# Kernel optimization log

Hardware: AMD Instinct MI355X
Metric: run time of the kernel (lower is better)

## Reference

```python
import jax, jax.numpy as jnp
import numpy as np

SQRT2 = np.float32(np.sqrt(2.0))


def _depthwise(x, h, axis):
    """Symmetric-pad depthwise 1D conv along `axis` (2=col/height, 3=row/width).
    Emulates dtcwt_slim ColFilter/RowFilter: prep_filt flips the taps, then
    F.conv2d cross-correlates with groups=C (same taps for every channel).
    x: (B,C,H,W), h: (L,) with L odd -> same-size output."""
    C = x.shape[1]
    L = h.shape[0]
    m = L // 2
    hf = jnp.flip(h)  # prep_filt stores h[::-1]
    if axis == 2:
        xp = jnp.pad(x, ((0, 0), (0, 0), (m, m), (0, 0)), mode='symmetric')
        ker = jnp.tile(hf[None, None, :, None], (C, 1, 1, 1))  # (C,1,L,1)
    else:
        xp = jnp.pad(x, ((0, 0), (0, 0), (0, 0), (m, m)), mode='symmetric')
        ker = jnp.tile(hf[None, None, None, :], (C, 1, 1, 1))  # (C,1,1,L)
    return jax.lax.conv_general_dilated(
        xp, ker, window_strides=(1, 1), padding='VALID',
        dimension_numbers=('NCHW', 'OIHW', 'NCHW'), feature_group_count=C)


def colfilter(x, h):
    return _depthwise(x, h, axis=2)


def rowfilter(x, h):
    return _depthwise(x, h, axis=3)


def c2q(w_r, w_i):
    """Complex pair of subbands -> real quad-interleaved image.
    w_r, w_i: (B,C,2,H,W) -> (B,C,2H,2W)."""
    w1r, w1i = w_r[:, :, 0], w_i[:, :, 0]
    w2r, w2i = w_r[:, :, 1], w_i[:, :, 1]
    x1 = w1r + w2r          # y[::2,  ::2]
    x2 = w1i + w2i          # y[::2, 1::2]
    x3 = w1i - w2i          # y[1::2, ::2]
    x4 = w2r - w1r          # y[1::2,1::2]
    B, C, H, W = x1.shape
    top = jnp.stack([x1, x2], axis=-1).reshape(B, C, H, 2 * W)
    bot = jnp.stack([x3, x4], axis=-1).reshape(B, C, H, 2 * W)
    y = jnp.stack([top, bot], axis=-2).reshape(B, C, 2 * H, 2 * W)
    return y / SQRT2


def setup_inputs() -> dict:
    key = jax.random.key(0)
    k1, k2, k3, k4, k5, k6 = jax.random.split(key, 6)
    B, C, H, W = 8, 64, 256, 256
    Yl = jax.random.normal(k1, (B, C, H, W), dtype=jnp.float32)
    Yhr = jax.random.normal(k2, (B, C, 6, H // 2, W // 2), dtype=jnp.float32)
    Yhi = jax.random.normal(k3, (B, C, 6, H // 2, W // 2), dtype=jnp.float32)
    # near_sym_b_bp synthesis filters (fixed, non-trainable buffers): 13/19/13 taps
    g0o = jax.random.normal(k4, (13,), dtype=jnp.float32) * 0.3
    g1o = jax.random.normal(k5, (19,), dtype=jnp.float32) * 0.3
    g2o = jax.random.normal(k6, (13,), dtype=jnp.float32) * 0.3
    return {"Yl": Yl, "Yhr": Yhr, "Yhi": Yhi, "g0o": g0o, "g1o": g1o, "g2o": g2o}


def reference(Yl, Yhr, Yhi, g0o, g1o, g2o):
    # orientation pairs: (15,165)->lh uses bands 0,5; (75,105)->hl bands 2,3;
    # (45,135 bandpass)->hh bands 1,4
    lh = c2q(Yhr[:, :, 0:6:5], Yhi[:, :, 0:6:5])
    hl = c2q(Yhr[:, :, 2:4:1], Yhi[:, :, 2:4:1])
    hh = c2q(Yhr[:, :, 1:5:3], Yhi[:, :, 1:5:3])
    y1 = colfilter(Yl, g0o) + colfilter(lh, g1o)
    y2 = colfilter(hl, g0o)
    y2bp = colfilter(hh, g2o)
    y = rowfilter(y1, g0o) + rowfilter(y2, g1o) + rowfilter(y2bp, g2o)
    return y
```

## Files before the change

### kernel.cpp

```cpp
#include <hip/hip_runtime.h>

#define PW 90
#define IS2 0.70710678118654752f

__device__ __forceinline__ int symidx(int t, int n) {
    t = (t < 0) ? (-1 - t) : t;
    return (t >= n) ? (2 * n - 1 - t) : t;
}

#define SB() __builtin_amdgcn_sched_barrier(0)

__device__ __forceinline__ void col13_yl(
    float (&acc)[32], const float* __restrict__ ylp,
    const float* __restrict__ taps, int r0, int cc)
{
    #pragma unroll
    for (int pi = 0; pi < 44; ++pi) {
        int rr = symidx(r0 - 6 + pi, 256);
        float v = ylp[rr * 256 + cc];
        #pragma unroll
        for (int j = 0; j < 13; ++j) {
            int ro = pi + j - 12;
            if (ro >= 0 && ro < 32) acc[ro] = fmaf(taps[j], v, acc[ro]);
        }
    }
}

__device__ __forceinline__ void col13_c2q(
    float (&acc)[32], const float* __restrict__ yhr, const float* __restrict__ yhi,
    int bA, int bB, const float* __restrict__ taps, int r0, int cc)
{
    const int cp = cc & 1;
    const int j2 = cc >> 1;
    #pragma unroll
    for (int pi = 0; pi < 44; ++pi) {
        int rr = symidx(r0 - 6 + pi, 256);
        int rp = rr & 1;
        int i2 = rr >> 1;
        const float* base = (((rp ^ cp) != 0) ? yhi : yhr) + (i2 * 128 + j2);
        float A  = base[bA * 16384];
        float Bv = base[bB * 16384];
        float vA = (rp & cp)       ? -A  : A;
        float vB = (rp & (cp ^ 1)) ? -Bv : Bv;
        float v = (vA + vB) * IS2;
        #pragma unroll
        for (int j = 0; j < 13; ++j) {
            int ro = pi + j - 12;
            if (ro >= 0 && ro < 32) acc[ro] = fmaf(taps[j], v, acc[ro]);
        }
    }
}

__device__ __forceinline__ void col19_c2q(
    float (&acc)[32], const float* __restrict__ yhr, const float* __restrict__ yhi,
    const float* __restrict__ taps, int r0, int cc)
{
    const int bA = 0, bB = 5;
    const int cp = cc & 1;
    const int j2 = cc >> 1;
    #pragma unroll
    for (int pi = 0; pi < 50; ++pi) {
        int rr = symidx(r0 - 9 + pi, 256);
        int rp = rr & 1;
        int i2 = rr >> 1;
        const float* base = (((rp ^ cp) != 0) ? yhi : yhr) + (i2 * 128 + j2);
        float A  = base[bA * 16384];
        float Bv = base[bB * 16384];
        float vA = (rp & cp)       ? -A  : A;
        float vB = (rp & (cp ^ 1)) ? -Bv : Bv;
        float v = (vA + vB) * IS2;
        #pragma unroll
        for (int j = 0; j < 19; ++j) {
            int ro = pi + j - 18;
            if (ro >= 0 && ro < 32) acc[ro] = fmaf(taps[j], v, acc[ro]);
        }
    }
}

template<int NU>
__device__ __forceinline__ void load_pairs(float (&buf)[28],
    const float* __restrict__ pEA, const float* __restrict__ pEB,
    const float* __restrict__ pOA, const float* __restrict__ pOB,
    int vof)
{
    #pragma unroll
    for (int u = 0; u < NU; ++u) {
        buf[4*u+0] = pEA[vof + u * 128];
        buf[4*u+1] = pEB[vof + u * 128];
        buf[4*u+2] = pOA[vof + u * 128];
        buf[4*u+3] = pOB[vof + u * 128];
    }
}

template<int L, int EPI0, int UB, int NU>
__device__ __forceinline__ void consume_pairs(float (&acc)[32], const float (&buf)[28],
                                              float sgn, const float* __restrict__ taps)
{
    #pragma unroll
    for (int u = 0; u < NU; ++u) {
        float ve = (buf[4*u+0] + buf[4*u+1]) * IS2;
        float vo = (buf[4*u+2] - buf[4*u+3]) * sgn;
        const int pi = EPI0 + 2 * (UB + u);
        #pragma unroll
        for (int j = 0; j < L; ++j) {
            int ro = pi + j - (L - 1);
            if (ro >= 0 && ro < 32) acc[ro] = fmaf(taps[j], ve, acc[ro]);
        }
        #pragma unroll
        for (int j = 0; j < L; ++j) {
            int ro = pi + 1 + j - (L - 1);
            if (ro >= 0 && ro < 32) acc[ro] = fmaf(taps[j], vo, acc[ro]);
        }
    }
}

template<int NT>
__device__ __forceinline__ void load_rows(float (&buf)[11], const float* __restrict__ p, int t0)
{
    #pragma unroll
    for (int t = 0; t < NT; ++t) buf[t] = p[(t0 + t) * 256];
}

template<int TB, int NT>
__device__ __forceinline__ void consume_rows(float (&acc)[32], const float (&buf)[11],
                                             const float* __restrict__ taps)
{
    #pragma unroll
    for (int t = 0; t < NT; ++t) {
        float v = buf[t];
        const int pi = TB + t;
        #pragma unroll
        for (int j = 0; j < 13; ++j) {
            int ro = pi + j - 12;
            if (ro >= 0 && ro < 32) acc[ro] = fmaf(taps[j], v, acc[ro]);
        }
    }
}

template<int L, int EPI0, int NPT, int C>
__device__ __forceinline__ void c2q_col_pipe(
    float (&acc)[32],
    const float* __restrict__ pEA, const float* __restrict__ pEB,
    const float* __restrict__ pOA, const float* __restrict__ pOB,
    int vof, float sgn, const float* __restrict__ taps)
{
    float bufA[28], bufB[28];
    constexpr int R = NPT - 3 * C;
    load_pairs<C>(bufA, pEA, pEB, pOA, pOB, vof);
    SB();
    load_pairs<C>(bufB, pEA, pEB, pOA, pOB, vof + C * 128);
    SB();
    consume_pairs<L, EPI0, 0, C>(acc, bufA, sgn, taps);
    SB();
    load_pairs<C>(bufA, pEA, pEB, pOA, pOB, vof + 2 * C * 128);
    SB();
    consume_pairs<L, EPI0, C, C>(acc, bufB, sgn, taps);
    SB();
    load_pairs<R>(bufB, pEA, pEB, pOA, pOB, vof + 3 * C * 128);
    SB();
    consume_pairs<L, EPI0, 2 * C, C>(acc, bufA, sgn, taps);
    SB();
    consume_pairs<L, EPI0, 3 * C, R>(acc, bufB, sgn, taps);
}

extern "C" __global__ __launch_bounds__(512, 4) void dtcwt_inv(
    const float* __restrict__ Yl, const float* __restrict__ Yhr,
    const float* __restrict__ Yhi,
    const float* __restrict__ g0, const float* __restrict__ g1,
    const float* __restrict__ g2, float* __restrict__ out)
{
    __shared__ __align__(16) float sU[3][32][PW];

    const int tid = threadIdx.x;
    const int wg  = blockIdx.x;
    const int swz = (wg & 7) * 2048 + (wg >> 3);
    const int plane = swz >> 5;
    const int bt = swz & 31;
    const int bx = bt & 3;
    const int by = bt >> 2;
    const int r0 = by * 32;
    const int c0 = bx * 64;

    const float* ylp = Yl  + (size_t)plane * 65536;
    const float* yhr = Yhr + (size_t)plane * 6 * 16384;
    const float* yhi = Yhi + (size_t)plane * 6 * 16384;

    const bool rowInterior = (by >= 1) && (by <= 6);

    const int role = tid >> 7;
    const int lr   = tid & 127;

    float acc[32];
    #pragma unroll
    for (int i = 0; i < 32; ++i) acc[i] = 0.0f;
    int ti = -1;

    if (rowInterior) {
        if (role == 0) {
            if (lr < 76) {
                ti = lr + 6;
                int cc = symidx(c0 + lr - 6, 256);
                const float* p = ylp + (r0 - 6) * 256 + cc;
                float bufA[11], bufB[11];
                load_rows<11>(bufA, p, 0);
                SB();
                load_rows<11>(bufB, p, 11);
                SB();
                consume_rows<0, 11>(acc, bufA, g0);
                SB();
                load_rows<11>(bufA, p, 22);
                SB();
                consume_rows<11, 11>(acc, bufB, g0);
                SB();
                load_rows<11>(bufB, p, 33);
                SB();
                consume_rows<22, 11>(acc, bufA, g0);
                SB();
                consume_rows<33, 11>(acc, bufB, g0);
            }
        } else if (role == 1) {
            if (lr < 76) {
                ti = lr + 6;
                int cc = symidx(c0 + lr - 6, 256);
                int cp = cc & 1, j2 = cc >> 1;
                const float* pE = cp ? yhi : yhr;
                const float* pO = cp ? yhr : yhi;
                float sgn = cp ? -IS2 : IS2;
                int vof = ((r0 - 10) >> 1) * 128 + j2;
                c2q_col_pipe<19, -1, 26, 7>(acc,
                    pE + 0 * 16384, pE + 5 * 16384,
                    pO + 0 * 16384, pO + 5 * 16384, vof, sgn, g1);
            }
        } else if (role == 2) {
            if (lr < 82) {
                ti = lr + 3;
                int cc = symidx(c0 + lr - 9, 256);
                int cp = cc & 1, j2 = cc >> 1;
                const float* pE = cp ? yhi : yhr;
                const float* pO = cp ? yhr : yhi;
                float sgn = cp ? -IS2 : IS2;
                int vof = ((r0 - 6) >> 1) * 128 + j2;
                c2q_col_pipe<13, 0, 22, 6>(acc,
                    pE + 2 * 16384, pE + 3 * 16384,
                    pO + 2 * 16384, pO + 3 * 16384, vof, sgn, g0);
            }
        } else {
            if (lr < 76) {
                ti = lr + 6;
                int cc = symidx(c0 + lr - 6, 256);
                int cp = cc & 1, j2 = cc >> 1;
                const float* pE = cp ? yhi : yhr;
                const float* pO = cp ? yhr : yhi;
                float sgn = cp ? -IS2 : IS2;
                int vof = ((r0 - 6) >> 1) * 128 + j2;
                c2q_col_pipe<13, 0, 22, 6>(acc,
                    pE + 1 * 16384, pE + 4 * 16384,
                    pO + 1 * 16384, pO + 4 * 16384, vof, sgn, g2);
            }
        }
    } else {
        if (role == 0) {
            if (lr < 76) {
                ti = lr + 6;
                int cc = symidx(c0 + ti - 12, 256);
                col13_yl(acc, ylp, g0, r0, cc);
            }
        } else if (role == 1) {
            if (lr < 76) {
                ti = lr + 6;
                int cc = symidx(c0 + ti - 12, 256);
                col19_c2q(acc, yhr, yhi, g1, r0, cc);
            }
        } else if (role == 2) {
            if (lr < 82) {
                ti = lr + 3;
                int cc = symidx(c0 + ti - 12, 256);
                col13_c2q(acc, yhr, yhi, 2, 3, g0, r0, cc);
            }
        } else {
            if (lr < 76) {
                ti = lr + 6;
                int cc = symidx(c0 + ti - 12, 256);
                col13_c2q(acc, yhr, yhi, 1, 4, g2, r0, cc);
            }
        }
    }

    if (ti >= 0 && role != 1) {
        const int bi = (role == 0) ? 0 : (role == 2 ? 1 : 2);
        #pragma unroll
        for (int ro = 0; ro < 32; ++ro) sU[bi][ro][ti] = acc[ro];
    }
    __syncthreads();

    if (role == 1 && ti >= 0) {
        #pragma unroll
        for (int ro = 0; ro < 32; ++ro) sU[0][ro][ti] += acc[ro];
    }

    const int cg = tid & 15;
    const int r2 = tid >> 4;
    const int cb = 4 * cg;

    float w2[28];
    #pragma unroll
    for (int k = 0; k < 14; ++k) {
        float2 a = *(const float2*)&sU[1][r2][cb + 2 * k];
        w2[2*k] = a.x; w2[2*k+1] = a.y;
    }
    float w3[20];
    #pragma unroll
    for (int k = 0; k < 10; ++k) {
        float2 a = *(const float2*)&sU[2][r2][cb + 4 + 2 * k];
        w3[2*k] = a.x; w3[2*k+1] = a.y;
    }
    __syncthreads();

    float w1[20];
    #pragma unroll
    for (int k = 0; k < 10; ++k) {
        float2 a = *(const float2*)&sU[0][r2][cb + 4 + 2 * k];
        w1[2*k] = a.x; w1[2*k+1] = a.y;
    }

    float4 res;
    float* op = (float*)&res;
    #pragma unroll
    for (int q = 0; q < 4; ++q) {
        float s = 0.0f;
        #pragma unroll
        for (int j = 0; j < 13; ++j) s = fmaf(g0[j], w1[q + 14 - j], s);
        #pragma unroll
        for (int j = 0; j < 19; ++j) s = fmaf(g1[j], w2[q + 21 - j], s);
        #pragma unroll
        for (int j = 0; j < 13; ++j) s = fmaf(g2[j], w3[q + 14 - j], s);
        op[q] = s;
    }
    *(float4*)&out[(size_t)plane * 65536 + (size_t)(r0 + r2) * 256 + (c0 + cb)] = res;
}

extern "C" void kernel_launch(void* const* d_in, const int* in_sizes, int n_in,
                              void* d_out, int out_size, void* d_ws, size_t ws_size,
                              hipStream_t stream) {
    const float* Yl  = (const float*)d_in[0];
    const float* Yhr = (const float*)d_in[1];
    const float* Yhi = (const float*)d_in[2];
    const float* g0  = (const float*)d_in[3];
    const float* g1  = (const float*)d_in[4];
    const float* g2  = (const float*)d_in[5];
    float* out = (float*)d_out;

    dim3 grid(16384, 1, 1);
    dim3 block(512, 1, 1);
    dtcwt_inv<<<grid, block, 0, stream>>>(Yl, Yhr, Yhi, g0, g1, g2, out);
}
```

Baseline: 312.6 us.

## Shrink tiles to 32x32, split 19-tap column pass across two waves

Output tiles shrink from 32x64 to 32x32, so the grid doubles and blocks drop from 512 to 320 threads, five 64-lane waves with one subband role each. The 19-tap lh column filter is split by input row range across two waves, which merge their partials into shared memory with atomicAdd. Shared buffers are resized per subband. The aim is better lane utilisation and balance across waves, at the cost of more halo recomputation per output pixel and idle threads in the row pass.

```diff
diff --git a/kernel.cpp b/kernel.cpp
--- a/kernel.cpp
+++ b/kernel.cpp
@@ -1,6 +1,7 @@
 #include <hip/hip_runtime.h>
 
-#define PW 90
+#define P1 46
+#define P2 52
 #define IS2 0.70710678118654752f
 
 __device__ __forceinline__ int symidx(int t, int n) {
@@ -51,21 +52,21 @@
     }
 }
 
-__device__ __forceinline__ void col19_c2q(
+template<int PI0, int PI1>
+__device__ __forceinline__ void col19_c2q_rng(
     float (&acc)[32], const float* __restrict__ yhr, const float* __restrict__ yhi,
     const float* __restrict__ taps, int r0, int cc)
 {
-    const int bA = 0, bB = 5;
     const int cp = cc & 1;
     const int j2 = cc >> 1;
     #pragma unroll
-    for (int pi = 0; pi < 50; ++pi) {
+    for (int pi = PI0; pi < PI1; ++pi) {
         int rr = symidx(r0 - 9 + pi, 256);
         int rp = rr & 1;
         int i2 = rr >> 1;
         const float* base = (((rp ^ cp) != 0) ? yhi : yhr) + (i2 * 128 + j2);
-        float A  = base[bA * 16384];
-        float Bv = base[bB * 16384];
+        float A  = base[0 * 16384];
+        float Bv = base[5 * 16384];
         float vA = (rp & cp)       ? -A  : A;
         float vB = (rp & (cp ^ 1)) ? -Bv : Bv;
         float v = (vA + vB) * IS2;
@@ -78,7 +79,7 @@
 }
 
 template<int NU>
-__device__ __forceinline__ void load_pairs(float (&buf)[28],
+__device__ __forceinline__ void load_pairs(float* buf,
     const float* __restrict__ pEA, const float* __restrict__ pEB,
     const float* __restrict__ pOA, const float* __restrict__ pOB,
     int vof)
@@ -93,7 +94,7 @@
 }
 
 template<int L, int EPI0, int UB, int NU>
-__device__ __forceinline__ void consume_pairs(float (&acc)[32], const float (&buf)[28],
+__device__ __forceinline__ void consume_pairs(float (&acc)[32], const float* buf,
                                               float sgn, const float* __restrict__ taps)
 {
     #pragma unroll
@@ -114,72 +115,75 @@
     }
 }
 
-template<int NT>
-__device__ __forceinline__ void load_rows(float (&buf)[11], const float* __restrict__ p, int t0)
-{
-    #pragma unroll
-    for (int t = 0; t < NT; ++t) buf[t] = p[(t0 + t) * 256];
-}
-
-template<int TB, int NT>
-__device__ __forceinline__ void consume_rows(float (&acc)[32], const float (&buf)[11],
-                                             const float* __restrict__ taps)
-{
-    #pragma unroll
-    for (int t = 0; t < NT; ++t) {
-        float v = buf[t];
-        const int pi = TB + t;
-        #pragma unroll
-        for (int j = 0; j < 13; ++j) {
-            int ro = pi + j - 12;
-            if (ro >= 0 && ro < 32) acc[ro] = fmaf(taps[j], v, acc[ro]);
-        }
-    }
-}
-
-template<int L, int EPI0, int NPT, int C>
+template<int L, int EPI0, int UOFF, int NPT, int C>
 __device__ __forceinline__ void c2q_col_pipe(
     float (&acc)[32],
     const float* __restrict__ pEA, const float* __restrict__ pEB,
     const float* __restrict__ pOA, const float* __restrict__ pOB,
     int vof, float sgn, const float* __restrict__ taps)
 {
-    float bufA[28], bufB[28];
+    float bufA[4 * C], bufB[4 * C];
     constexpr int R = NPT - 3 * C;
+    static_assert(R > 0 && R <= C, "chunking");
     load_pairs<C>(bufA, pEA, pEB, pOA, pOB, vof);
     SB();
     load_pairs<C>(bufB, pEA, pEB, pOA, pOB, vof + C * 128);
     SB();
-    consume_pairs<L, EPI0, 0, C>(acc, bufA, sgn, taps);
+    consume_pairs<L, EPI0, UOFF + 0, C>(acc, bufA, sgn, taps);
     SB();
     load_pairs<C>(bufA, pEA, pEB, pOA, pOB, vof + 2 * C * 128);
     SB();
-    consume_pairs<L, EPI0, C, C>(acc, bufB, sgn, taps);
+    consume_pairs<L, EPI0, UOFF + C, C>(acc, bufB, sgn, taps);
     SB();
     load_pairs<R>(bufB, pEA, pEB, pOA, pOB, vof + 3 * C * 128);
     SB();
-    consume_pairs<L, EPI0, 2 * C, C>(acc, bufA, sgn, taps);
-    SB();
-    consume_pairs<L, EPI0, 3 * C, R>(acc, bufB, sgn, taps);
-}
-
-extern "C" __global__ __launch_bounds__(512, 4) void dtcwt_inv(
+    consume_pairs<L, EPI0, UOFF + 2 * C, C>(acc, bufA, sgn, taps);
+    SB();
+    consume_pairs<L, EPI0, UOFF + 3 * C, R>(acc, bufB, sgn, taps);
+}
+
+template<int NT>
+__device__ __forceinline__ void load_rows(float (&buf)[11], const float* __restrict__ p, int t0)
+{
+    #pragma unroll
+    for (int t = 0; t < NT; ++t) buf[t] = p[(t0 + t) * 256];
+}
+
+template<int TB, int NT>
+__device__ __forceinline__ void consume_rows(float (&acc)[32], const float (&buf)[11],
+                                             const float* __restrict__ taps)
+{
+    #pragma unroll
+    for (int t = 0; t < NT; ++t) {
+        float v = buf[t];
+        const int pi = TB + t;
+        #pragma unroll
+        for (int j = 0; j < 13; ++j) {
+            int ro = pi + j - 12;
+            if (ro >= 0 && ro < 32) acc[ro] = fmaf(taps[j], v, acc[ro]);
+        }
+    }
+}
+
+extern "C" __global__ __launch_bounds__(320, 4) void dtcwt_inv(
     const float* __restrict__ Yl, const float* __restrict__ Yhr,
     const float* __restrict__ Yhi,
     const float* __restrict__ g0, const float* __restrict__ g1,
     const float* __restrict__ g2, float* __restrict__ out)
 {
-    __shared__ __align__(16) float sU[3][32][PW];
+    __shared__ __align__(16) float sU1[32][P1];
+    __shared__ __align__(16) float sU2[32][P2];
+    __shared__ __align__(16) float sU3[32][P1];
 
     const int tid = threadIdx.x;
     const int wg  = blockIdx.x;
-    const int swz = (wg & 7) * 2048 + (wg >> 3);
-    const int plane = swz >> 5;
-    const int bt = swz & 31;
-    const int bx = bt & 3;
-    const int by = bt >> 2;
+    const int swz = (wg & 7) * 4096 + (wg >> 3);
+    const int plane = swz >> 6;
+    const int bt = swz & 63;
+    const int bx = bt & 7;
+    const int by = bt >> 3;
     const int r0 = by * 32;
-    const int c0 = bx * 64;
+    const int c0 = bx * 32;
 
     const float* ylp = Yl  + (size_t)plane * 65536;
     const float* yhr = Yhr + (size_t)plane * 6 * 16384;
@@ -187,19 +191,19 @@
 
     const bool rowInterior = (by >= 1) && (by <= 6);
 
-    const int role = tid >> 7;
-    const int lr   = tid & 127;
+    const int w    = tid >> 6;
+    const int lane = tid & 63;
 
     float acc[32];
     #pragma unroll
     for (int i = 0; i < 32; ++i) acc[i] = 0.0f;
-    int ti = -1;
-
-    if (rowInterior) {
-        if (role == 0) {
-            if (lr < 76) {
-                ti = lr + 6;
-                int cc = symidx(c0 + lr - 6, 256);
+
+    bool lhAct = false;
+
+    if (w == 0) {
+        if (lane < 44) {
+            int cc = symidx(c0 - 6 + lane, 256);
+            if (rowInterior) {
                 const float* p = ylp + (r0 - 6) * 256 + cc;
                 float bufA[11], bufB[11];
                 load_rows<11>(bufA, p, 0);
@@ -217,126 +221,121 @@
                 consume_rows<22, 11>(acc, bufA, g0);
                 SB();
                 consume_rows<33, 11>(acc, bufB, g0);
+            } else {
+                col13_yl(acc, ylp, g0, r0, cc);
             }
-        } else if (role == 1) {
-            if (lr < 76) {
-                ti = lr + 6;
-                int cc = symidx(c0 + lr - 6, 256);
+            #pragma unroll
+            for (int ro = 0; ro < 32; ++ro) sU1[ro][lane] = acc[ro];
+        }
+    } else if (w == 1 || w == 2) {
+        if (lane < 44) {
+            lhAct = true;
+            int cc = symidx(c0 - 6 + lane, 256);
+            if (rowInterior) {
                 int cp = cc & 1, j2 = cc >> 1;
                 const float* pE = cp ? yhi : yhr;
                 const float* pO = cp ? yhr : yhi;
                 float sgn = cp ? -IS2 : IS2;
                 int vof = ((r0 - 10) >> 1) * 128 + j2;
-                c2q_col_pipe<19, -1, 26, 7>(acc,
-                    pE + 0 * 16384, pE + 5 * 16384,
-                    pO + 0 * 16384, pO + 5 * 16384, vof, sgn, g1);
+                if (w == 1)
+                    c2q_col_pipe<19, -1, 0, 13, 4>(acc,
+                        pE + 0 * 16384, pE + 5 * 16384,
+                        pO + 0 * 16384, pO + 5 * 16384, vof, sgn, g1);
+                else
+                    c2q_col_pipe<19, -1, 13, 13, 4>(acc,
+                        pE + 0 * 16384, pE + 5 * 16384,
+                        pO + 0 * 16384, pO + 5 * 16384, vof + 13 * 128, sgn, g1);
+            } else {
+                if (w == 1) col19_c2q_rng<0, 25>(acc, yhr, yhi, g1, r0, cc);
+                else        col19_c2q_rng<25, 50>(acc, yhr, yhi, g1, r0, cc);
             }
-        } else if (role == 2) {
-            if (lr < 82) {
-                ti = lr + 3;
-                int cc = symidx(c0 + lr - 9, 256);
+        }
+    } else if (w == 3) {
+        if (lane < 50) {
+            int cc = symidx(c0 - 9 + lane, 256);
+            if (rowInterior) {
                 int cp = cc & 1, j2 = cc >> 1;
                 const float* pE = cp ? yhi : yhr;
                 const float* pO = cp ? yhr : yhi;
                 float sgn = cp ? -IS2 : IS2;
                 int vof = ((r0 - 6) >> 1) * 128 + j2;
-                c2q_col_pipe<13, 0, 22, 6>(acc,
+                c2q_col_pipe<13, 0, 0, 22, 6>(acc,
                     pE + 2 * 16384, pE + 3 * 16384,
                     pO + 2 * 16384, pO + 3 * 16384, vof, sgn, g0);
+            } else {
+                col13_c2q(acc, yhr, yhi, 2, 3, g0, r0, cc);
             }
-        } else {
-            if (lr < 76) {
-                ti = lr + 6;
-                int cc = symidx(c0 + lr - 6, 256);
+            #pragma unroll
+            for (int ro = 0; ro < 32; ++ro) sU2[ro][lane] = acc[ro];
+        }
+    } else {
+        if (lane < 44) {
+            int cc = symidx(c0 - 6 + lane, 256);
+            if (rowInterior) {
                 int cp = cc & 1, j2 = cc >> 1;
                 const float* pE = cp ? yhi : yhr;
                 const float* pO = cp ? yhr : yhi;
                 float sgn = cp ? -IS2 : IS2;
                 int vof = ((r0 - 6) >> 1) * 128 + j2;
-                c2q_col_pipe<13, 0, 22, 6>(acc,
+                c2q_col_pipe<13, 0, 0, 22, 6>(acc,
                     pE + 1 * 16384, pE + 4 * 16384,
                     pO + 1 * 16384, pO + 4 * 16384, vof, sgn, g2);
-            }
-        }
-    } else {
-        if (role == 0) {
-            if (lr < 76) {
-                ti = lr + 6;
-                int cc = symidx(c0 + ti - 12, 256);
-                col13_yl(acc, ylp, g0, r0, cc);
-            }
-        } else if (role == 1) {
-            if (lr < 76) {
-                ti = lr + 6;
-                int cc = symidx(c0 + ti - 12, 256);
-                col19_c2q(acc, yhr, yhi, g1, r0, cc);
-            }
-        } else if (role == 2) {
-            if (lr < 82) {
-                ti = lr + 3;
-                int cc = symidx(c0 + ti - 12, 256);
-                col13_c2q(acc, yhr, yhi, 2, 3, g0, r0, cc);
-            }
-        } else {
-            if (lr < 76) {
-                ti = lr + 6;
-                int cc = symidx(c0 + ti - 12, 256);
+            } else {
                 col13_c2q(acc, yhr, yhi, 1, 4, g2, r0, cc);
             }
-        }
-    }
-
-    if (ti >= 0 && role != 1) {
-        const int bi = (role == 0) ? 0 : (role == 2 ? 1 : 2);
-        #pragma unroll
-        for (int ro = 0; ro < 32; ++ro) sU[bi][ro][ti] = acc[ro];
+            #pragma unroll
+            for (int ro = 0; ro < 32; ++ro) sU3[ro][lane] = acc[ro];
+        }
     }
     __syncthreads();
 
-    if (role == 1 && ti >= 0) {
-        #pragma unroll
-        for (int ro = 0; ro < 32; ++ro) sU[0][ro][ti] += acc[ro];
-    }
-
-    const int cg = tid & 15;
-    const int r2 = tid >> 4;
+    if (lhAct) {
+        #pragma unroll
+        for (int ro = 0; ro < 32; ++ro) atomicAdd(&sU1[ro][lane], acc[ro]);
+    }
+
+    const int r2 = (tid & 255) >> 3;
+    const int cg = tid & 7;
     const int cb = 4 * cg;
 
-    float w2[28];
-    #pragma unroll
-    for (int k = 0; k < 14; ++k) {
-        float2 a = *(const float2*)&sU[1][r2][cb + 2 * k];
-        w2[2*k] = a.x; w2[2*k+1] = a.y;
-    }
-    float w3[20];
-    #pragma unroll
-    for (int k = 0; k < 10; ++k) {
-        float2 a = *(const float2*)&sU[2][r2][cb + 4 + 2 * k];
-        w3[2*k] = a.x; w3[2*k+1] = a.y;
+    float w2v[22], w3v[16];
+    if (tid < 256) {
+        #pragma unroll
+        for (int k = 0; k < 11; ++k) {
+            float2 a = *(const float2*)&sU2[r2][cb + 2 * k];
+            w2v[2*k] = a.x; w2v[2*k+1] = a.y;
+        }
+        #pragma unroll
+        for (int k = 0; k < 8; ++k) {
+            float2 a = *(const float2*)&sU3[r2][cb + 2 * k];
+            w3v[2*k] = a.x; w3v[2*k+1] = a.y;
+        }
     }
     __syncthreads();
 
-    float w1[20];
-    #pragma unroll
-    for (int k = 0; k < 10; ++k) {
-        float2 a = *(const float2*)&sU[0][r2][cb + 4 + 2 * k];
-        w1[2*k] = a.x; w1[2*k+1] = a.y;
-    }
-
-    float4 res;
-    float* op = (float*)&res;
-    #pragma unroll
-    for (int q = 0; q < 4; ++q) {
-        float s = 0.0f;
-        #pragma unroll
-        for (int j = 0; j < 13; ++j) s = fmaf(g0[j], w1[q + 14 - j], s);
-        #pragma unroll
-        for (int j = 0; j < 19; ++j) s = fmaf(g1[j], w2[q + 21 - j], s);
-        #pragma unroll
-        for (int j = 0; j < 13; ++j) s = fmaf(g2[j], w3[q + 14 - j], s);
-        op[q] = s;
-    }
-    *(float4*)&out[(size_t)plane * 65536 + (size_t)(r0 + r2) * 256 + (c0 + cb)] = res;
+    if (tid < 256) {
+        float w1v[16];
+        #pragma unroll
+        for (int k = 0; k < 8; ++k) {
+            float2 a = *(const float2*)&sU1[r2][cb + 2 * k];
+            w1v[2*k] = a.x; w1v[2*k+1] = a.y;
+        }
+
+        float4 res;
+        float* op = (float*)&res;
+        #pragma unroll
+        for (int q = 0; q < 4; ++q) {
+            float s = 0.0f;
+            #pragma unroll
+            for (int j = 0; j < 13; ++j) s = fmaf(g0[j], w1v[q + 12 - j], s);
+            #pragma unroll
+            for (int j = 0; j < 19; ++j) s = fmaf(g1[j], w2v[q + 18 - j], s);
+            #pragma unroll
+            for (int j = 0; j < 13; ++j) s = fmaf(g2[j], w3v[q + 12 - j], s);
+            op[q] = s;
+        }
+        *(float4*)&out[(size_t)plane * 65536 + (size_t)(r0 + r2) * 256 + (c0 + cb)] = res;
+    }
 }
 
 extern "C" void kernel_launch(void* const* d_in, const int* in_sizes, int n_in,
@@ -350,7 +349,7 @@
     const float* g2  = (const float*)d_in[5];
     float* out = (float*)d_out;
 
-    dim3 grid(16384, 1, 1);
-    dim3 block(512, 1, 1);
+    dim3 grid(32768, 1, 1);
+    dim3 block(320, 1, 1);
     dtcwt_inv<<<grid, block, 0, stream>>>(Yl, Yhr, Yhi, g0, g1, g2, out);
 }
```

New measurement: 763.4 us. 2.44x slower.
